# Kernel tuning notes

Hardware: AMD Instinct MI355X
Metric: run time of the kernel (lower is better)

Reference implementation:

```python
import jax, jax.numpy as jnp
import numpy as np

K = 32          # k_value
NUM_CLASSES = 10


def setup_inputs() -> dict:
    key = jax.random.key(0)
    k1, k2, k3 = jax.random.split(key, 3)
    queries = jax.random.normal(k1, (1024, 64), dtype=jnp.float32)
    train_data = jax.random.normal(k2, (200000, 64), dtype=jnp.float32)
    train_labels = jax.random.randint(k3, (200000,), 0, NUM_CLASSES, dtype=jnp.int32)
    return {"queries": queries, "train_data": train_data, "train_labels": train_labels}


def _votes(queries, train_data, train_labels):
    # Squared Euclidean distance [Q, N] via the ||q||^2 + ||x||^2 - 2 q.x expansion
    # (same math as sum of squared differences, O(Q*N*d) without a Q*N*d temp).
    q2 = jnp.sum(queries * queries, axis=1, keepdims=True)        # [Q, 1]
    x2 = jnp.sum(train_data * train_data, axis=1)                  # [N]
    sim = q2 + x2[None, :] - 2.0 * (queries @ train_data.T)        # [Q, N]
    sim = jnp.maximum(sim, 0.0)  # exact squared distances are >= 0
    # Inversion kernel: replace exact zeros with 0.1, then weights = 1/sim.
    sim = jnp.where(sim == 0.0, jnp.float32(0.1), sim)
    weights = 1.0 / sim                                            # [Q, N]
    # Top-K weights (largest weight == nearest neighbor).
    top_w, top_i = jax.lax.top_k(weights, K)                       # [Q, K]
    top_lab = train_labels[top_i]                                  # [Q, K] int
    # segment_sum over labels == scatter-add weights per class.
    Q = queries.shape[0]
    rows = jnp.arange(Q)[:, None]                                  # [Q, 1]
    votes = jnp.zeros((Q, NUM_CLASSES), dtype=top_w.dtype).at[rows, top_lab].add(top_w)
    return votes


def reference(queries, train_data, train_labels):
    votes = _votes(queries, train_data, train_labels)
    # argmax over class weight sums == tf.argmax(segment_sum) per query
    return jnp.argmax(votes, axis=1)
```

## Files before the change

kernel.cpp:

```cpp
#include <hip/hip_runtime.h>
#include <hip/hip_bf16.h>

#define N_TRAIN 200000
#define DIMS    64
#define NQ      1024
#define KSEL    32
#define NCLS    10

#define CHROWS2 391
#define NBLK0   512
#define LCAP    8
#define OVFCAP  256
#define TOTC    4096
#define MAXS    1536
#define SAMPLES 8192
#define NPB     3125

typedef float f32x4 __attribute__((ext_vector_type(4)));
typedef short bf16x8 __attribute__((ext_vector_type(8)));

__device__ __forceinline__ unsigned fmap(float f) {
    unsigned u = __float_as_uint(f);
    return u ^ ((u >> 31) ? 0xFFFFFFFFu : 0x80000000u);
}
__device__ __forceinline__ float funmap(unsigned m) {
    unsigned u = m ^ ((m >> 31) ? 0x80000000u : 0xFFFFFFFFu);
    return __uint_as_float(u);
}
__device__ __forceinline__ unsigned short f2bf(float f) {
    unsigned u = __float_as_uint(f);
    unsigned r = u + 0x7FFFu + ((u >> 16) & 1u);
    return (unsigned short)(r >> 16);
}
__device__ __forceinline__ bf16x8 pack8(float4 a, float4 b) {
    bf16x8 r;
    r[0] = (short)f2bf(a.x); r[1] = (short)f2bf(a.y);
    r[2] = (short)f2bf(a.z); r[3] = (short)f2bf(a.w);
    r[4] = (short)f2bf(b.x); r[5] = (short)f2bf(b.y);
    r[6] = (short)f2bf(b.z); r[7] = (short)f2bf(b.w);
    return r;
}

__global__ __launch_bounds__(512) void k_prep(const float* __restrict__ X,
                                              float* __restrict__ x2,
                                              float* __restrict__ bmax,
                                              short* __restrict__ Xb) {
    int T = blockIdx.x * 512 + threadIdx.x;
    int row = T >> 3;
    int l8 = T & 7;
    const float4* xp = (const float4*)(X + (long)row * 64 + l8 * 8);
    float4 a = xp[0], b = xp[1];
    *(bf16x8*)(Xb + (long)row * 64 + l8 * 8) = pack8(a, b);
    float p = a.x * a.x + a.y * a.y + a.z * a.z + a.w * a.w +
              b.x * b.x + b.y * b.y + b.z * b.z + b.w * b.w;
    p += __shfl_xor(p, 1);
    p += __shfl_xor(p, 2);
    p += __shfl_xor(p, 4);
    if (l8 == 0) x2[row] = p;
    float m = p;
    m = fmaxf(m, __shfl_xor(m, 8));
    m = fmaxf(m, __shfl_xor(m, 16));
    m = fmaxf(m, __shfl_xor(m, 32));
    __shared__ float wm[8];
    if ((threadIdx.x & 63) == 0) wm[threadIdx.x >> 6] = m;
    __syncthreads();
    if (threadIdx.x == 0) {
        float r = wm[0];
#pragma unroll
        for (int i = 1; i < 8; i++) r = fmaxf(r, wm[i]);
        bmax[blockIdx.x] = r;
    }
}

__global__ __launch_bounds__(256) void k_max(const float* __restrict__ bmax,
                                             float* __restrict__ x2maxf) {
    float m = -1e30f;
    for (int i = threadIdx.x; i < NPB; i += 256) m = fmaxf(m, bmax[i]);
#pragma unroll
    for (int d = 1; d < 64; d <<= 1) m = fmaxf(m, __shfl_xor(m, d));
    __shared__ float wm[4];
    if ((threadIdx.x & 63) == 0) wm[threadIdx.x >> 6] = m;
    __syncthreads();
    if (threadIdx.x == 0)
        *x2maxf = fmaxf(fmaxf(wm[0], wm[1]), fmaxf(wm[2], wm[3]));
}

__global__ __launch_bounds__(256) void k_cvt(const float* __restrict__ src,
                                             short* __restrict__ dst) {
    long c = (long)blockIdx.x * 256 + threadIdx.x;
    const float4* xp = (const float4*)(src + c * 8);
    float4 a = xp[0], b = xp[1];
    *(bf16x8*)(dst + c * 8) = pack8(a, b);
}

template<int MODE>
__global__ __launch_bounds__(512) void k_dist(
    const short* __restrict__ Xb, const short* __restrict__ Qb,
    const float* __restrict__ x2, const float* __restrict__ tqw,
    unsigned* __restrict__ pcnt, unsigned* __restrict__ pool,
    unsigned* __restrict__ ovfcnt, uint2* __restrict__ ovf,
    unsigned short* __restrict__ keys) {
    int bid = blockIdx.x;
    int tid = threadIdx.x;
    int qt = tid >> 6;
    int lane = tid & 63;
    int lr = lane & 15;
    int lk = lane >> 4;

    __shared__ short xs[128 * 64];
    __shared__ float x2s[128];
    __shared__ unsigned lcnt[MODE == 0 ? NQ : 1];
    __shared__ unsigned lbuf[MODE == 0 ? NQ * LCAP : 1];

    int r0 = MODE ? (bid << 7) : bid * CHROWS2;
    int rowEnd = MODE ? (r0 + 128) : min(r0 + CHROWS2, N_TRAIN);
    int rcnt = rowEnd - r0;

    if (MODE == 0) { lcnt[tid] = 0u; lcnt[tid + 512] = 0u; }

    bf16x8 afr[8][2];
#pragma unroll
    for (int qi = 0; qi < 8; qi++) {
        const short* qp = Qb + (long)((qt << 7) + (qi << 4) + lr) * 64 + (lk << 3);
        afr[qi][0] = *(const bf16x8*)qp;
        afr[qi][1] = *(const bf16x8*)(qp + 32);
    }
    float htq[8];
    if (MODE == 0) {
#pragma unroll
        for (int qi = 0; qi < 8; qi++) {
            float4 t4 = *(const float4*)(tqw + (qt << 7) + (qi << 4) + (lk << 2));
            htq[qi] = 0.5f * fmaxf(fmaxf(t4.x, t4.y), fmaxf(t4.z, t4.w));
        }
    }

    for (int sb = 0; sb < rcnt; sb += 128) {
        __syncthreads();
#pragma unroll
        for (int k = 0; k < 2; k++) {
            int c = tid + (k << 9);
            int r = c >> 3, sl = c & 7;
            bf16x8 v = *(const bf16x8*)(Xb + (long)(r0 + sb + r) * 64 + ((sl ^ (r & 7)) << 3));
            *(bf16x8*)(xs + r * 64 + (sl << 3)) = v;
        }
        if (tid < 128) x2s[tid] = x2[r0 + sb + tid];
        __syncthreads();

#pragma unroll
        for (int g16 = 0; g16 < 8; g16++) {
            int r = (g16 << 4) + lr;
            int grow = r0 + sb + r;
            bool valid = grow < rowEnd;
            int sw = r & 7;
            bf16x8 b0 = *(const bf16x8*)(xs + r * 64 + ((lk ^ sw) << 3));
            bf16x8 b1 = *(const bf16x8*)(xs + r * 64 + (((4 + lk) ^ sw) << 3));
            float x2c = x2s[r];
            float hx = 0.5f * x2c;
#pragma unroll
            for (int qi = 0; qi < 8; qi++) {
                f32x4 acc = {0.f, 0.f, 0.f, 0.f};
                acc = __builtin_amdgcn_mfma_f32_16x16x32_bf16(afr[qi][0], b0, acc, 0, 0, 0);
                acc = __builtin_amdgcn_mfma_f32_16x16x32_bf16(afr[qi][1], b1, acc, 0, 0, 0);
                if (MODE == 1) {
#pragma unroll
                    for (int r4 = 0; r4 < 4; r4++) {
                        unsigned k16 = fmap(x2c - 2.f * acc[r4]) >> 16;
                        unsigned o = (unsigned)__shfl_xor((int)k16, 1);
                        unsigned v2 = k16 | (o << 16);
                        unsigned p2 = (unsigned)__shfl_xor((int)v2, 2);
                        if ((lr & 3) == 0) {
                            int qg = (qt << 7) + (qi << 4) + (lk << 2) + r4;
                            *(uint2*)(&keys[(long)qg * SAMPLES + grow]) = make_uint2(v2, p2);
                        }
                    }
                } else {
                    float mx = fmaxf(fmaxf(acc[0], acc[1]), fmaxf(acc[2], acc[3]));
                    if (valid && mx + htq[qi] >= hx) {
                        float4 t4 = *(const float4*)(tqw + (qt << 7) + (qi << 4) + (lk << 2));
                        float tq4[4] = {t4.x, t4.y, t4.z, t4.w};
#pragma unroll
                        for (int r4 = 0; r4 < 4; r4++) {
                            if (acc[r4] + 0.5f * tq4[r4] >= hx) {
                                int qg = (qt << 7) + (qi << 4) + (lk << 2) + r4;
                                unsigned key16 = fmap(x2c - 2.f * acc[r4]) >> 16;
                                unsigned slot = atomicAdd(&lcnt[qg], 1u);
                                if (slot < LCAP) {
                                    lbuf[qg * LCAP + slot] = (key16 << 9) | (unsigned)(grow - r0);
                                } else {
                                    unsigned o = atomicAdd(&ovfcnt[qg], 1u);
                                    if (o < OVFCAP)
                                        ovf[qg * OVFCAP + o] = make_uint2(key16, (unsigned)grow);
                                }
                            }
                        }
                    }
                }
            }
        }
    }

    if (MODE == 0) {
        __syncthreads();
        for (int q = tid; q < NQ; q += 512) {
            unsigned lc = min(lcnt[q], (unsigned)LCAP);
            pcnt[(bid << 10) + q] = lc;
            uint4 a = *(uint4*)&lbuf[q * LCAP];
            uint4 b = *(uint4*)&lbuf[q * LCAP + 4];
            long base = ((long)(bid << 10) + q) * LCAP;
            *(uint4*)&pool[base] = a;
            *(uint4*)&pool[base + 4] = b;
        }
    }
}

__global__ __launch_bounds__(256) void k_sel(const unsigned short* __restrict__ keys,
                                             const float* __restrict__ Qm,
                                             const float* __restrict__ x2maxf,
                                             float* __restrict__ tqw,
                                             float* __restrict__ q2g) {
    int q = blockIdx.x, tid = threadIdx.x;
    unsigned short mk[32];
#pragma unroll
    for (int m = 0; m < 32; m++) mk[m] = keys[(long)q * SAMPLES + tid + 256 * m];
    __shared__ float q2s_;
    __shared__ int cnt;
    if (tid < 64) {
        float v = Qm[(long)q * 64 + tid];
        float p = v * v;
#pragma unroll
        for (int d = 1; d < 64; d <<= 1) p += __shfl_xor(p, d);
        if (tid == 0) q2s_ = p;
    }
    unsigned lo = 0, hi = 65535;
    for (int it = 0; it < 16; ++it) {
        __syncthreads();
        if (tid == 0) cnt = 0;
        __syncthreads();
        unsigned mid = (lo + hi) >> 1;
        int c = 0;
#pragma unroll
        for (int m = 0; m < 32; m++) c += (mk[m] <= mid) ? 1 : 0;
#pragma unroll
        for (int d = 1; d < 64; d <<= 1) c += __shfl_xor(c, d);
        if ((tid & 63) == 0) atomicAdd(&cnt, c);
        __syncthreads();
        if (cnt >= KSEL) hi = mid; else lo = mid + 1;
    }
    if (tid == 0) {
        unsigned vv = hi + 2u; if (vv > 65535u) vv = 65535u;
        float t = funmap(vv << 16);
        float q2 = q2s_;
        tqw[q] = t + 0.0314f * sqrtf(q2 * (*x2maxf)) + 0.2f;
        q2g[q] = q2;
    }
}

__global__ __launch_bounds__(256) void k_merge(const float* __restrict__ Qm,
                                               const float* __restrict__ X,
                                               const float* __restrict__ x2,
                                               const int* __restrict__ labels,
                                               const unsigned* __restrict__ pcnt,
                                               const unsigned* __restrict__ pool,
                                               const unsigned* __restrict__ ovfcnt,
                                               const uint2* __restrict__ ovf,
                                               const float* __restrict__ q2g,
                                               const float* __restrict__ x2maxf,
                                               int* __restrict__ out) {
    int q = blockIdx.x, tid = threadIdx.x;
    __shared__ unsigned short eK[TOTC];
    __shared__ int eR[TOTC];
    __shared__ int sR[MAXS];
    __shared__ float sKey[MAXS];
    __shared__ int sLab[MAXS];
    __shared__ float qs[64];
    __shared__ int tot, cnt, ns, nw, nt;
    __shared__ unsigned cutS;
    __shared__ float wKey[34];
    __shared__ int wLab[34];
    __shared__ int tIdx[64];
    __shared__ int tLab[64];

    if (tid == 0) { tot = 0; ns = 0; nw = 0; nt = 0; }
    if (tid < 64) qs[tid] = Qm[(long)q * 64 + tid];
    __syncthreads();

    for (int b = tid; b < NBLK0; b += 256) {
        unsigned lc = pcnt[(b << 10) + q];
        if (lc) {
            long base = ((long)(b << 10) + q) * LCAP;
            uint4 a = *(const uint4*)&pool[base];
            uint4 bb = *(const uint4*)&pool[base + 4];
            int p = atomicAdd(&tot, (int)lc);
            int rbase = b * CHROWS2;
#pragma unroll
            for (int i = 0; i < LCAP; i++) {
                unsigned e = (i == 0) ? a.x : (i == 1) ? a.y : (i == 2) ? a.z :
                             (i == 3) ? a.w : (i == 4) ? bb.x : (i == 5) ? bb.y :
                             (i == 6) ? bb.z : bb.w;
                int p2 = p + i;
                if ((unsigned)i < lc && p2 < TOTC) {
                    eK[p2] = (unsigned short)(e >> 9);
                    eR[p2] = rbase + (int)(e & 511u);
                }
            }
        }
    }
    int ov = min((int)ovfcnt[q], OVFCAP);
    for (int i = tid; i < ov; i += 256) {
        uint2 e = ovf[q * OVFCAP + i];
        int p = atomicAdd(&tot, 1);
        if (p < TOTC) { eK[p] = (unsigned short)e.x; eR[p] = (int)e.y; }
    }
    __syncthreads();
    int T = min(tot, TOTC);

    unsigned short mk[16];
#pragma unroll
    for (int m = 0; m < 16; m++) { int i = tid + (m << 8); mk[m] = (i < T) ? eK[i] : (unsigned short)0xFFFFu; }
    unsigned lo = 0, hi = 65535;
    for (int it = 0; it < 16; ++it) {
        __syncthreads();
        if (tid == 0) cnt = 0;
        __syncthreads();
        unsigned mid = (lo + hi) >> 1;
        int c = 0;
#pragma unroll
        for (int m = 0; m < 16; m++) c += (mk[m] <= mid) ? 1 : 0;
#pragma unroll
        for (int d = 1; d < 64; d <<= 1) c += __shfl_xor(c, d);
        if ((tid & 63) == 0) atomicAdd(&cnt, c);
        __syncthreads();
        if (cnt >= KSEL) hi = mid; else lo = mid + 1;
    }
    float q2v = q2g[q];
    if (tid == 0) {
        unsigned vv = min(hi + 1u, 65535u);
        float tf = funmap(vv << 16);
        float err = 0.0314f * sqrtf(q2v * (*x2maxf)) + 0.3f;
        cutS = min((fmap(tf + err) >> 16) + 1u, 65535u);
    }
    __syncthreads();
    unsigned cut = cutS;
    for (int i = tid; i < T; i += 256)
        if ((unsigned)eK[i] <= cut) { int p = atomicAdd(&ns, 1); if (p < MAXS) sR[p] = eR[i]; }
    __syncthreads();
    int NS = min(ns, MAXS);

    for (int i = tid; i < NS; i += 256) {
        int row = sR[i];
        const float4* xr = (const float4*)(X + (long)row * 64);
        const float4* qr = (const float4*)qs;
        float dot = 0.f;
#pragma unroll
        for (int k4 = 0; k4 < 16; k4++) {
            float4 xv = xr[k4], qv = qr[k4];
            dot += qv.x * xv.x + qv.y * xv.y + qv.z * xv.z + qv.w * xv.w;
        }
        sKey[i] = x2[row] - 2.f * dot;
        sLab[i] = labels[row];
    }
    __syncthreads();

    unsigned uk[6];
#pragma unroll
    for (int m = 0; m < 6; m++) { int i = tid + (m << 8); uk[m] = (i < NS) ? fmap(sKey[i]) : 0xFFFFFFFFu; }
    unsigned lo2 = 0u, hi2 = 0xFFFFFFFFu;
    for (int it = 0; it < 32; ++it) {
        __syncthreads();
        if (tid == 0) cnt = 0;
        __syncthreads();
        unsigned mid = lo2 + ((hi2 - lo2) >> 1);
        int c = 0;
#pragma unroll
        for (int m = 0; m < 6; m++) c += (uk[m] <= mid) ? 1 : 0;
#pragma unroll
        for (int d = 1; d < 64; d <<= 1) c += __shfl_xor(c, d);
        if ((tid & 63) == 0) atomicAdd(&cnt, c);
        __syncthreads();
        if (cnt >= KSEL) hi2 = mid; else lo2 = mid + 1;
    }
    unsigned T32 = hi2;

#pragma unroll
    for (int m = 0; m < 6; m++) {
        int i = tid + (m << 8);
        if (i < NS) {
            if (uk[m] < T32) {
                int p = atomicAdd(&nw, 1);
                if (p < 34) { wKey[p] = sKey[i]; wLab[p] = sLab[i]; }
            } else if (uk[m] == T32) {
                int p = atomicAdd(&nt, 1);
                if (p < 64) { tIdx[p] = sR[i]; tLab[p] = sLab[i]; }
            }
        }
    }
    __syncthreads();

    if (tid == 0) {
        float votes[NCLS] = {0.f, 0.f, 0.f, 0.f, 0.f, 0.f, 0.f, 0.f, 0.f, 0.f};
        int NW = min(nw, 32);
        for (int i = 0; i < NW; i++) {
            float dist = q2v + wKey[i];
            if (dist < 0.f) dist = 0.f;
            if (dist == 0.f) dist = 0.1f;
            votes[wLab[i]] += 1.f / dist;
        }
        int need = KSEL - NW;
        int NT = min(nt, 64);
        float tkey = funmap(T32);
        float dist = q2v + tkey;
        if (dist < 0.f) dist = 0.f;
        if (dist == 0.f) dist = 0.1f;
        float twgt = 1.f / dist;
        for (int t = 0; t < need && t < NT; t++) {
            int best = -1, bi = 0x7FFFFFFF;
            for (int u = 0; u < NT; u++)
                if (tIdx[u] < bi) { bi = tIdx[u]; best = u; }
            if (best < 0) break;
            votes[tLab[best]] += twgt;
            tIdx[best] = 0x7FFFFFFF;
        }
        float bv = votes[0];
        int bc = 0;
#pragma unroll
        for (int c = 1; c < NCLS; c++)
            if (votes[c] > bv) { bv = votes[c]; bc = c; }
        out[q] = bc;
    }
}

extern "C" void kernel_launch(void* const* d_in, const int* in_sizes, int n_in,
                              void* d_out, int out_size, void* d_ws, size_t ws_size,
                              hipStream_t stream) {
    const float* Qm = (const float*)d_in[0];
    const float* X = (const float*)d_in[1];
    const int* labels = (const int*)d_in[2];
    char* ws = (char*)d_ws;
    float* x2 = (float*)(ws + 0);
    float* tqw = (float*)(ws + 800000);
    float* q2g = (float*)(ws + 804096);
    float* x2maxf = (float*)(ws + 808192);
    float* bmax = (float*)(ws + 808256);
    unsigned* pcnt = (unsigned*)(ws + 820800);
    unsigned* ovfcnt = (unsigned*)(ws + 2917952);
    uint2* ovf = (uint2*)(ws + 2922048);
    unsigned short* keys = (unsigned short*)(ws + 5019200);
    unsigned* pool = (unsigned*)(ws + 5019200);
    short* Xb = (short*)(ws + 21796416);
    short* Qb = (short*)(ws + 47396416);
    int* out = (int*)d_out;

    hipMemsetAsync(ovfcnt, 0, 4096, stream);
    k_prep<<<NPB, 512, 0, stream>>>(X, x2, bmax, Xb);
    k_max<<<1, 256, 0, stream>>>(bmax, x2maxf);
    k_cvt<<<32, 256, 0, stream>>>(Qm, Qb);
    k_dist<1><<<SAMPLES / 128, 512, 0, stream>>>(Xb, Qb, x2, tqw, pcnt, pool, ovfcnt, ovf, keys);
    k_sel<<<NQ, 256, 0, stream>>>(keys, Qm, x2maxf, tqw, q2g);
    k_dist<0><<<NBLK0, 512, 0, stream>>>(Xb, Qb, x2, tqw, pcnt, pool, ovfcnt, ovf, keys);
    k_merge<<<NQ, 256, 0, stream>>>(Qm, X, x2, labels, pcnt, pool, ovfcnt, ovf, q2g, x2maxf, out);
}
```

Measured before the change: 302.8 us.

## Switch distance MFMA to fp16, drop LDS staging, tighten candidate error bounds

Converts the training and query data to fp16 instead of bf16 and uses the f16 MFMA. The extra mantissa precision lets the candidate thresholds shrink (error coefficient 0.0314 down to 0.004, additive 0.3/0.2 down to 0.1), so fewer candidates should pass the filter and the merge stage does less exact rescoring. The distance kernel now loads B fragments straight from global memory with no shared-memory tile, and the sampling pass uses 32-row blocks, giving more blocks. Merge keys widen from 16 to 23 bits, which needs a longer bisection loop and more shared memory. fp16 could overflow or lose range for large inputs, and the tighter bounds lean on fp16 accuracy.

Measured after the change: 244.6 us. -19.2%, faster.

```diff
diff --git a/kernel.cpp b/kernel.cpp
--- a/kernel.cpp
+++ b/kernel.cpp
@@ -1,5 +1,6 @@
 #include <hip/hip_runtime.h>
 #include <hip/hip_bf16.h>
+#include <hip/hip_fp16.h>
 
 #define N_TRAIN 200000
 #define DIMS    64
@@ -14,10 +15,11 @@
 #define TOTC    4096
 #define MAXS    1536
 #define SAMPLES 8192
+#define SROWS   32
 #define NPB     3125
 
 typedef float f32x4 __attribute__((ext_vector_type(4)));
-typedef short bf16x8 __attribute__((ext_vector_type(8)));
+typedef short f16x8 __attribute__((ext_vector_type(8)));
 
 __device__ __forceinline__ unsigned fmap(float f) {
     unsigned u = __float_as_uint(f);
@@ -27,30 +29,30 @@
     unsigned u = m ^ ((m >> 31) ? 0x80000000u : 0xFFFFFFFFu);
     return __uint_as_float(u);
 }
-__device__ __forceinline__ unsigned short f2bf(float f) {
-    unsigned u = __float_as_uint(f);
-    unsigned r = u + 0x7FFFu + ((u >> 16) & 1u);
-    return (unsigned short)(r >> 16);
-}
-__device__ __forceinline__ bf16x8 pack8(float4 a, float4 b) {
-    bf16x8 r;
-    r[0] = (short)f2bf(a.x); r[1] = (short)f2bf(a.y);
-    r[2] = (short)f2bf(a.z); r[3] = (short)f2bf(a.w);
-    r[4] = (short)f2bf(b.x); r[5] = (short)f2bf(b.y);
-    r[6] = (short)f2bf(b.z); r[7] = (short)f2bf(b.w);
+__device__ __forceinline__ unsigned short f2h(float f) {
+    union { __half h; unsigned short u; } c;
+    c.h = __float2half_rn(f);
+    return c.u;
+}
+__device__ __forceinline__ f16x8 pack8h(float4 a, float4 b) {
+    f16x8 r;
+    r[0] = (short)f2h(a.x); r[1] = (short)f2h(a.y);
+    r[2] = (short)f2h(a.z); r[3] = (short)f2h(a.w);
+    r[4] = (short)f2h(b.x); r[5] = (short)f2h(b.y);
+    r[6] = (short)f2h(b.z); r[7] = (short)f2h(b.w);
     return r;
 }
 
 __global__ __launch_bounds__(512) void k_prep(const float* __restrict__ X,
                                               float* __restrict__ x2,
                                               float* __restrict__ bmax,
-                                              short* __restrict__ Xb) {
+                                              short* __restrict__ Xh) {
     int T = blockIdx.x * 512 + threadIdx.x;
     int row = T >> 3;
     int l8 = T & 7;
     const float4* xp = (const float4*)(X + (long)row * 64 + l8 * 8);
     float4 a = xp[0], b = xp[1];
-    *(bf16x8*)(Xb + (long)row * 64 + l8 * 8) = pack8(a, b);
+    *(f16x8*)(Xh + (long)row * 64 + l8 * 8) = pack8h(a, b);
     float p = a.x * a.x + a.y * a.y + a.z * a.z + a.w * a.w +
               b.x * b.x + b.y * b.y + b.z * b.z + b.w * b.w;
     p += __shfl_xor(p, 1);
@@ -90,12 +92,12 @@
     long c = (long)blockIdx.x * 256 + threadIdx.x;
     const float4* xp = (const float4*)(src + c * 8);
     float4 a = xp[0], b = xp[1];
-    *(bf16x8*)(dst + c * 8) = pack8(a, b);
+    *(f16x8*)(dst + c * 8) = pack8h(a, b);
 }
 
 template<int MODE>
 __global__ __launch_bounds__(512) void k_dist(
-    const short* __restrict__ Xb, const short* __restrict__ Qb,
+    const short* __restrict__ Xh, const short* __restrict__ Qh,
     const float* __restrict__ x2, const float* __restrict__ tqw,
     unsigned* __restrict__ pcnt, unsigned* __restrict__ pool,
     unsigned* __restrict__ ovfcnt, uint2* __restrict__ ovf,
@@ -107,23 +109,24 @@
     int lr = lane & 15;
     int lk = lane >> 4;
 
-    __shared__ short xs[128 * 64];
-    __shared__ float x2s[128];
     __shared__ unsigned lcnt[MODE == 0 ? NQ : 1];
     __shared__ unsigned lbuf[MODE == 0 ? NQ * LCAP : 1];
 
-    int r0 = MODE ? (bid << 7) : bid * CHROWS2;
-    int rowEnd = MODE ? (r0 + 128) : min(r0 + CHROWS2, N_TRAIN);
-    int rcnt = rowEnd - r0;
-
-    if (MODE == 0) { lcnt[tid] = 0u; lcnt[tid + 512] = 0u; }
-
-    bf16x8 afr[8][2];
+    int r0 = MODE ? (bid * SROWS) : bid * CHROWS2;
+    int rowEnd = MODE ? (r0 + SROWS) : min(r0 + CHROWS2, N_TRAIN);
+
+    if (MODE == 0) {
+        lcnt[tid] = 0u;
+        lcnt[tid + 512] = 0u;
+        __syncthreads();
+    }
+
+    f16x8 afr[8][2];
 #pragma unroll
     for (int qi = 0; qi < 8; qi++) {
-        const short* qp = Qb + (long)((qt << 7) + (qi << 4) + lr) * 64 + (lk << 3);
-        afr[qi][0] = *(const bf16x8*)qp;
-        afr[qi][1] = *(const bf16x8*)(qp + 32);
+        const short* qp = Qh + (long)((qt << 7) + (qi << 4) + lr) * 64 + (lk << 3);
+        afr[qi][0] = *(const f16x8*)qp;
+        afr[qi][1] = *(const f16x8*)(qp + 32);
     }
     float htq[8];
     if (MODE == 0) {
@@ -134,63 +137,52 @@
         }
     }
 
-    for (int sb = 0; sb < rcnt; sb += 128) {
-        __syncthreads();
-#pragma unroll
-        for (int k = 0; k < 2; k++) {
-            int c = tid + (k << 9);
-            int r = c >> 3, sl = c & 7;
-            bf16x8 v = *(const bf16x8*)(Xb + (long)(r0 + sb + r) * 64 + ((sl ^ (r & 7)) << 3));
-            *(bf16x8*)(xs + r * 64 + (sl << 3)) = v;
-        }
-        if (tid < 128) x2s[tid] = x2[r0 + sb + tid];
-        __syncthreads();
-
-#pragma unroll
-        for (int g16 = 0; g16 < 8; g16++) {
-            int r = (g16 << 4) + lr;
-            int grow = r0 + sb + r;
-            bool valid = grow < rowEnd;
-            int sw = r & 7;
-            bf16x8 b0 = *(const bf16x8*)(xs + r * 64 + ((lk ^ sw) << 3));
-            bf16x8 b1 = *(const bf16x8*)(xs + r * 64 + (((4 + lk) ^ sw) << 3));
-            float x2c = x2s[r];
-            float hx = 0.5f * x2c;
-#pragma unroll
-            for (int qi = 0; qi < 8; qi++) {
-                f32x4 acc = {0.f, 0.f, 0.f, 0.f};
-                acc = __builtin_amdgcn_mfma_f32_16x16x32_bf16(afr[qi][0], b0, acc, 0, 0, 0);
-                acc = __builtin_amdgcn_mfma_f32_16x16x32_bf16(afr[qi][1], b1, acc, 0, 0, 0);
-                if (MODE == 1) {
+    for (int base = r0; base < rowEnd; base += 16) {
+        int row = base + lr;
+        bool valid = row < rowEnd;
+        int rowc = valid ? row : (rowEnd - 1);
+        const short* xp = Xh + (long)rowc * 64 + (lk << 3);
+        f16x8 b0 = *(const f16x8*)xp;
+        f16x8 b1 = *(const f16x8*)(xp + 32);
+        float x2c = valid ? x2[rowc] : 1e30f;
+        float hx = 0.5f * x2c;
+
+#pragma unroll
+        for (int qi = 0; qi < 8; qi++) {
+            f32x4 acc = {0.f, 0.f, 0.f, 0.f};
+            acc = __builtin_amdgcn_mfma_f32_16x16x32_f16(afr[qi][0], b0, acc, 0, 0, 0);
+            acc = __builtin_amdgcn_mfma_f32_16x16x32_f16(afr[qi][1], b1, acc, 0, 0, 0);
+            if (MODE == 1) {
+#pragma unroll
+                for (int r4 = 0; r4 < 4; r4++) {
+                    unsigned k16 = fmap(x2c - 2.f * acc[r4]) >> 16;
+                    unsigned o = (unsigned)__shfl_xor((int)k16, 1);
+                    unsigned v2 = k16 | (o << 16);
+                    unsigned p2 = (unsigned)__shfl_xor((int)v2, 2);
+                    if ((lr & 3) == 0) {
+                        int qg = (qt << 7) + (qi << 4) + (lk << 2) + r4;
+                        *(uint2*)(&keys[(long)qg * SAMPLES + row]) = make_uint2(v2, p2);
+                    }
+                }
+            } else {
+                float mx = fmaxf(fmaxf(acc[0], acc[1]), fmaxf(acc[2], acc[3]));
+                if (valid && mx + htq[qi] >= hx) {
+                    float4 t4 = *(const float4*)(tqw + (qt << 7) + (qi << 4) + (lk << 2));
+                    float tq4[4] = {t4.x, t4.y, t4.z, t4.w};
 #pragma unroll
                     for (int r4 = 0; r4 < 4; r4++) {
-                        unsigned k16 = fmap(x2c - 2.f * acc[r4]) >> 16;
-                        unsigned o = (unsigned)__shfl_xor((int)k16, 1);
-                        unsigned v2 = k16 | (o << 16);
-                        unsigned p2 = (unsigned)__shfl_xor((int)v2, 2);
-                        if ((lr & 3) == 0) {
+                        if (acc[r4] + 0.5f * tq4[r4] >= hx) {
                             int qg = (qt << 7) + (qi << 4) + (lk << 2) + r4;
-                            *(uint2*)(&keys[(long)qg * SAMPLES + grow]) = make_uint2(v2, p2);
-                        }
-                    }
-                } else {
-                    float mx = fmaxf(fmaxf(acc[0], acc[1]), fmaxf(acc[2], acc[3]));
-                    if (valid && mx + htq[qi] >= hx) {
-                        float4 t4 = *(const float4*)(tqw + (qt << 7) + (qi << 4) + (lk << 2));
-                        float tq4[4] = {t4.x, t4.y, t4.z, t4.w};
-#pragma unroll
-                        for (int r4 = 0; r4 < 4; r4++) {
-                            if (acc[r4] + 0.5f * tq4[r4] >= hx) {
-                                int qg = (qt << 7) + (qi << 4) + (lk << 2) + r4;
-                                unsigned key16 = fmap(x2c - 2.f * acc[r4]) >> 16;
-                                unsigned slot = atomicAdd(&lcnt[qg], 1u);
-                                if (slot < LCAP) {
-                                    lbuf[qg * LCAP + slot] = (key16 << 9) | (unsigned)(grow - r0);
-                                } else {
-                                    unsigned o = atomicAdd(&ovfcnt[qg], 1u);
-                                    if (o < OVFCAP)
-                                        ovf[qg * OVFCAP + o] = make_uint2(key16, (unsigned)grow);
-                                }
+                            unsigned entry = (fmap(x2c - 2.f * acc[r4]) & 0xFFFFFE00u) |
+                                             (unsigned)(row - r0);
+                            unsigned slot = atomicAdd(&lcnt[qg], 1u);
+                            if (slot < LCAP) {
+                                lbuf[qg * LCAP + slot] = entry;
+                            } else {
+                                unsigned o = atomicAdd(&ovfcnt[qg], 1u);
+                                if (o < OVFCAP)
+                                    ovf[qg * OVFCAP + o] =
+                                        make_uint2(entry >> 9, (unsigned)row);
                             }
                         }
                     }
@@ -250,7 +242,7 @@
         unsigned vv = hi + 2u; if (vv > 65535u) vv = 65535u;
         float t = funmap(vv << 16);
         float q2 = q2s_;
-        tqw[q] = t + 0.0314f * sqrtf(q2 * (*x2maxf)) + 0.2f;
+        tqw[q] = t + 0.004f * sqrtf(q2 * (*x2maxf)) + 0.1f;
         q2g[q] = q2;
     }
 }
@@ -267,7 +259,7 @@
                                                const float* __restrict__ x2maxf,
                                                int* __restrict__ out) {
     int q = blockIdx.x, tid = threadIdx.x;
-    __shared__ unsigned short eK[TOTC];
+    __shared__ unsigned eK[TOTC];
     __shared__ int eR[TOTC];
     __shared__ int sR[MAXS];
     __shared__ float sKey[MAXS];
@@ -299,7 +291,7 @@
                              (i == 6) ? bb.z : bb.w;
                 int p2 = p + i;
                 if ((unsigned)i < lc && p2 < TOTC) {
-                    eK[p2] = (unsigned short)(e >> 9);
+                    eK[p2] = e >> 9;
                     eR[p2] = rbase + (int)(e & 511u);
                 }
             }
@@ -309,16 +301,16 @@
     for (int i = tid; i < ov; i += 256) {
         uint2 e = ovf[q * OVFCAP + i];
         int p = atomicAdd(&tot, 1);
-        if (p < TOTC) { eK[p] = (unsigned short)e.x; eR[p] = (int)e.y; }
+        if (p < TOTC) { eK[p] = e.x; eR[p] = (int)e.y; }
     }
     __syncthreads();
     int T = min(tot, TOTC);
 
-    unsigned short mk[16];
-#pragma unroll
-    for (int m = 0; m < 16; m++) { int i = tid + (m << 8); mk[m] = (i < T) ? eK[i] : (unsigned short)0xFFFFu; }
-    unsigned lo = 0, hi = 65535;
-    for (int it = 0; it < 16; ++it) {
+    unsigned mk[16];
+#pragma unroll
+    for (int m = 0; m < 16; m++) { int i = tid + (m << 8); mk[m] = (i < T) ? eK[i] : 0xFFFFFFFFu; }
+    unsigned lo = 0, hi = 0x7FFFFFu;
+    for (int it = 0; it < 23; ++it) {
         __syncthreads();
         if (tid == 0) cnt = 0;
         __syncthreads();
@@ -334,15 +326,15 @@
     }
     float q2v = q2g[q];
     if (tid == 0) {
-        unsigned vv = min(hi + 1u, 65535u);
-        float tf = funmap(vv << 16);
-        float err = 0.0314f * sqrtf(q2v * (*x2maxf)) + 0.3f;
-        cutS = min((fmap(tf + err) >> 16) + 1u, 65535u);
+        unsigned vv = min(hi + 1u, 0x7FFFFFu);
+        float tf = funmap(vv << 9);
+        float err = 0.004f * sqrtf(q2v * (*x2maxf)) + 0.1f;
+        cutS = min((fmap(tf + err) >> 9) + 1u, 0x7FFFFFu);
     }
     __syncthreads();
     unsigned cut = cutS;
     for (int i = tid; i < T; i += 256)
-        if ((unsigned)eK[i] <= cut) { int p = atomicAdd(&ns, 1); if (p < MAXS) sR[p] = eR[i]; }
+        if (eK[i] <= cut) { int p = atomicAdd(&ns, 1); if (p < MAXS) sR[p] = eR[i]; }
     __syncthreads();
     int NS = min(ns, MAXS);
 
@@ -446,16 +438,16 @@
     uint2* ovf = (uint2*)(ws + 2922048);
     unsigned short* keys = (unsigned short*)(ws + 5019200);
     unsigned* pool = (unsigned*)(ws + 5019200);
-    short* Xb = (short*)(ws + 21796416);
-    short* Qb = (short*)(ws + 47396416);
+    short* Xh = (short*)(ws + 21796416);
+    short* Qh = (short*)(ws + 47396416);
     int* out = (int*)d_out;
 
     hipMemsetAsync(ovfcnt, 0, 4096, stream);
-    k_prep<<<NPB, 512, 0, stream>>>(X, x2, bmax, Xb);
+    k_prep<<<NPB, 512, 0, stream>>>(X, x2, bmax, Xh);
     k_max<<<1, 256, 0, stream>>>(bmax, x2maxf);
-    k_cvt<<<32, 256, 0, stream>>>(Qm, Qb);
-    k_dist<1><<<SAMPLES / 128, 512, 0, stream>>>(Xb, Qb, x2, tqw, pcnt, pool, ovfcnt, ovf, keys);
+    k_cvt<<<32, 256, 0, stream>>>(Qm, Qh);
+    k_dist<1><<<SAMPLES / SROWS, 512, 0, stream>>>(Xh, Qh, x2, tqw, pcnt, pool, ovfcnt, ovf, keys);
     k_sel<<<NQ, 256, 0, stream>>>(keys, Qm, x2maxf, tqw, q2g);
-    k_dist<0><<<NBLK0, 512, 0, stream>>>(Xb, Qb, x2, tqw, pcnt, pool, ovfcnt, ovf, keys);
+    k_dist<0><<<NBLK0, 512, 0, stream>>>(Xh, Qh, x2, tqw, pcnt, pool, ovfcnt, ovf, keys);
     k_merge<<<NQ, 256, 0, stream>>>(Qm, X, x2, labels, pcnt, pool, ovfcnt, ovf, q2g, x2maxf, out);
 }
```
